# Optimization experiments

Measured on AMD Instinct MI355X. Metric: run time of the kernel, lower is better.

## Reference

```python
import jax, jax.numpy as jnp
import numpy as np

B, C, W, H = 2, 64, 96, 96  # N = W*H = 9216 spatial positions


def conv1x1(x, w, b):
    # x: (B, Cin, W, H), w: (Cout, Cin), b: (Cout,) -> (B, Cout, W, H)
    return jnp.einsum('bchw,oc->bohw', x, w) + b[None, :, None, None]


def setup_inputs() -> dict:
    key = jax.random.key(0)
    ks = jax.random.split(key, 4)
    c8 = C // 8
    s = 0.05  # small weight scale keeps softmax logits in a sane range
    return {
        'x': jax.random.normal(ks[0], (B, C, W, H), jnp.float32),
        'wq': jax.random.normal(ks[1], (c8, C), jnp.float32) * s,
        'bq': jnp.zeros((c8,), jnp.float32),
        'wk': jax.random.normal(ks[2], (c8, C), jnp.float32) * s,
        'bk': jnp.zeros((c8,), jnp.float32),
        'wv': jax.random.normal(ks[3], (C, C), jnp.float32) * s,
        'bv': jnp.zeros((C,), jnp.float32),
        'gamma': jnp.full((1,), 0.5, jnp.float32),
    }


def reference(x, wq, bq, wk, bk, wv, bv, gamma):
    b, c, w, h = x.shape
    n = w * h
    q = conv1x1(x, wq, bq).reshape(b, -1, n)   # (B, C//8, N)
    k = conv1x1(x, wk, bk).reshape(b, -1, n)   # (B, C//8, N)
    v = conv1x1(x, wv, bv).reshape(b, c, n)    # (B, C, N)
    energy = jnp.einsum('bci,bcj->bij', q, k)  # (B, N, N)
    attn = jax.nn.softmax(energy, axis=-1)
    # torch.bmm(v, attn): out[b,c,i] = sum_j v[b,c,j] * attn[b,j,i]
    out = jnp.einsum('bcj,bji->bci', v, attn).reshape(b, c, w, h)
    return gamma * out + x
```

## Files before the change

### kernel.cpp

```cpp
#include <hip/hip_runtime.h>

using half2v  = __attribute__((ext_vector_type(2))) _Float16;
using half4   = __attribute__((ext_vector_type(4))) _Float16;
using half8   = __attribute__((ext_vector_type(8))) _Float16;
using floatx4 = __attribute__((ext_vector_type(4))) float;

constexpr int BATCH = 2;
constexpr int NPOS  = 96 * 96;
constexpr int NT    = NPOS / 16;
constexpr int NST   = NPOS / 32;

#define EXP2(x) __builtin_amdgcn_exp2f(x)
#define MFMA16(A, B, C) __builtin_amdgcn_mfma_f32_16x16x16f16(A, B, C, 0, 0, 0)
#define MFMA32(A, B, C) __builtin_amdgcn_mfma_f32_16x16x32_f16(A, B, C, 0, 0, 0)

__device__ inline half8 p8_of(floatx4 e0, floatx4 e1) {
    half2v a0 = __builtin_bit_cast(half2v,
        __builtin_amdgcn_cvt_pkrtz(EXP2(e0[0]), EXP2(e0[1])));
    half2v a1 = __builtin_bit_cast(half2v,
        __builtin_amdgcn_cvt_pkrtz(EXP2(e0[2]), EXP2(e0[3])));
    half2v a2 = __builtin_bit_cast(half2v,
        __builtin_amdgcn_cvt_pkrtz(EXP2(e1[0]), EXP2(e1[1])));
    half2v a3 = __builtin_bit_cast(half2v,
        __builtin_amdgcn_cvt_pkrtz(EXP2(e1[2]), EXP2(e1[3])));
    half8 p = {a0[0], a0[1], a1[0], a1[1], a2[0], a2[1], a3[0], a3[1]};
    return p;
}

__global__ __launch_bounds__(256) void qkv_kernel(
    const float* __restrict__ x,
    const float* __restrict__ wq, const float* __restrict__ bq,
    const float* __restrict__ wk, const float* __restrict__ bk,
    const float* __restrict__ wv, const float* __restrict__ bv,
    _Float16* __restrict__ Qf, _Float16* __restrict__ Kf,
    _Float16* __restrict__ Vf)
{
    __shared__ float W[80][64];
    __shared__ float bias[80];
    __shared__ float qs[32][9];
    __shared__ float ks[32][9];
    __shared__ _Float16 vs[32][72];
    const int tid = threadIdx.x;
    for (int idx = tid; idx < 80 * 64; idx += 256) {
        int o = idx >> 6, c = idx & 63;
        float w;
        if (o < 8)       w = wq[o * 64 + c];
        else if (o < 16) w = wk[(o - 8) * 64 + c];
        else             w = wv[(o - 16) * 64 + c];
        W[o][c] = w;
    }
    if (tid < 80) {
        float bb;
        if (tid < 8)       bb = bq[tid];
        else if (tid < 16) bb = bk[tid - 8];
        else               bb = bv[tid - 16];
        bias[tid] = bb;
    }
    __syncthreads();

    const int js = blockIdx.x;
    const int b  = blockIdx.y;
    const int part = tid >> 5;
    const int jl   = tid & 31;
    const int i    = js * 32 + jl;

    float xr[64];
    #pragma unroll
    for (int c = 0; c < 64; ++c)
        xr[c] = x[(size_t)(b * 64 + c) * NPOS + i];

    #pragma unroll
    for (int q = 0; q < 10; ++q) {
        const int o = part * 10 + q;
        float s = bias[o];
        #pragma unroll
        for (int c4 = 0; c4 < 16; ++c4) {
            float4 w4 = *(const float4*)&W[o][c4 * 4];
            s += w4.x * xr[c4*4+0] + w4.y * xr[c4*4+1]
               + w4.z * xr[c4*4+2] + w4.w * xr[c4*4+3];
        }
        if (o < 8)       qs[jl][o] = s;
        else if (o < 16) ks[jl][o - 8] = s;
        else             vs[jl][o - 16] = (_Float16)s;
    }
    __syncthreads();

    const size_t tile = (size_t)b * NST + js;
    {
        const int ct = tid >> 6, l = tid & 63;
        const int g = l >> 4, cl = l & 15;
        half8 o8;
        #pragma unroll
        for (int idx = 0; idx < 8; ++idx)
            o8[idx] = vs[8 * g + idx][16 * ct + cl];
        *(half8*)&Vf[(tile * 256 + ct * 64 + l) * 8] = o8;
    }
    if (tid < 128) {
        const int l = tid >> 1, e = tid & 1;
        const int m = l & 15, g = l >> 4;
        const int jsrc = 8 * (m >> 2) + 4 * e + (m & 3);
        constexpr float LOG2E = 1.44269504088896f;
        half4 qh;
        #pragma unroll
        for (int r = 0; r < 4; ++r)
            qh[r] = (g < 2) ? (_Float16)(qs[jsrc][4 * g + r] * LOG2E)
                            : (_Float16)0.f;
        ((half4*)Qf)[(tile * 64 + l) * 2 + e] = qh;
    } else {
        const int t = tid - 128;
        const int ht = t >> 6, l = t & 63;
        const int il = l & 15, g = l >> 4;
        const int it = js * 2 + ht;
        half4 kh;
        #pragma unroll
        for (int r = 0; r < 4; ++r) {
            if (g < 2)       kh[r] = (_Float16)ks[16 * ht + il][4 * g + r];
            else if (g == 2) kh[r] = (r < 2) ? (_Float16)1.f : (_Float16)0.f;
            else             kh[r] = (_Float16)0.f;
        }
        ((half4*)Kf)[(size_t)(b * NT + it) * 64 + l] = kh;
    }
}

__global__ __launch_bounds__(256, 4) void denom_kernel(
    _Float16* __restrict__ Qf, const _Float16* __restrict__ Kf)
{
    __shared__ float LpS[4][32];
    const int tid = threadIdx.x;
    const int w = tid >> 6, l = tid & 63;
    const int js = blockIdx.x;
    const int b  = blockIdx.y;
    const size_t tile = (size_t)b * NST + js;
    const half8* __restrict__ qfb = (const half8*)Qf + (size_t)b * NST * 64;
    const half4* __restrict__ kfb = (const half4*)Kf + (size_t)b * NT * 64;

    half8 qv = qfb[(size_t)js * 64 + l];
    half4 q0 = __builtin_shufflevector(qv, qv, 0, 1, 2, 3);
    half4 q1 = __builtin_shufflevector(qv, qv, 4, 5, 6, 7);

    float sum[2][4];
    #pragma unroll
    for (int e = 0; e < 2; ++e)
        #pragma unroll
        for (int r = 0; r < 4; ++r) sum[e][r] = 0.f;

    const floatx4 z = {0.f, 0.f, 0.f, 0.f};
    #define DACC(E0, E1) do { \
        _Pragma("unroll") \
        for (int r = 0; r < 4; ++r) { \
            sum[0][r] += EXP2(E0[r]); sum[1][r] += EXP2(E1[r]); } \
    } while (0)

    const half4* kp = kfb + (size_t)w * 64 + l;
    half4 kfA = kp[0];
    half4 kfB = kp[256];
    floatx4 eA0 = MFMA16(q0, kfA, z), eA1 = MFMA16(q1, kfA, z);
    floatx4 eB0, eB1;
    for (int k = 0; k < 71; ++k) {
        kfA = kp[(size_t)(2 * k + 2) * 256];
        eB0 = MFMA16(q0, kfB, z); eB1 = MFMA16(q1, kfB, z);
        DACC(eA0, eA1);
        kfB = kp[(size_t)(2 * k + 3) * 256];
        eA0 = MFMA16(q0, kfA, z); eA1 = MFMA16(q1, kfA, z);
        DACC(eB0, eB1);
    }
    eB0 = MFMA16(q0, kfB, z); eB1 = MFMA16(q1, kfB, z);
    DACC(eA0, eA1);
    DACC(eB0, eB1);
    #undef DACC

    #pragma unroll
    for (int e = 0; e < 2; ++e)
        #pragma unroll
        for (int r = 0; r < 4; ++r)
            #pragma unroll
            for (int m = 1; m < 16; m <<= 1)
                sum[e][r] += __shfl_xor(sum[e][r], m, 64);

    if ((l & 15) == 0) {
        const int g = l >> 4;
        #pragma unroll
        for (int e = 0; e < 2; ++e)
            #pragma unroll
            for (int r = 0; r < 4; ++r)
                LpS[w][8 * g + 4 * e + r] = sum[e][r];
    }
    __syncthreads();

    if (tid < 32) {
        const float L = LpS[0][tid] + LpS[1][tid] + LpS[2][tid] + LpS[3][tid];
        const float v = -__log2f(L);
        _Float16 hi = (_Float16)v;
        _Float16 lo = (_Float16)(v - (float)hi);
        const int m = 4 * (tid >> 3) + (tid & 3);
        const int e = (tid >> 2) & 1;
        half2v hl = {hi, lo};
        ((half2v*)Qf)[((tile * 64 + m + 32) * 2 + e) * 2] = hl;
    }
}

__global__ __launch_bounds__(256, 2) void attn_kernel(
    const _Float16* __restrict__ Qf, const _Float16* __restrict__ Kf,
    const _Float16* __restrict__ Vf,
    const float* __restrict__ x, const float* __restrict__ gamma,
    float* __restrict__ out)
{
    __shared__ float red[4][3][64][17];
    const int s = blockIdx.x;
    const int b   = s & 1;
    const int igl = s >> 1;
    const int tid = threadIdx.x;
    const int w = tid >> 6, l = tid & 63;
    const int it0 = igl * 3, i0 = igl * 48;

    const half8* __restrict__ qfb = (const half8*)Qf + (size_t)b * NST * 64;
    const half4* __restrict__ kfb = (const half4*)Kf + (size_t)b * NT * 64;
    const half8* __restrict__ vfb = (const half8*)Vf + (size_t)b * NST * 256;

    half4 kf[3];
    #pragma unroll
    for (int st = 0; st < 3; ++st) kf[st] = kfb[(size_t)(it0 + st) * 64 + l];

    floatx4 acc[3][4];
    #pragma unroll
    for (int st = 0; st < 3; ++st)
        #pragma unroll
        for (int ct = 0; ct < 4; ++ct)
            acc[st][ct] = (floatx4){0.f, 0.f, 0.f, 0.f};

    const floatx4 z = {0.f, 0.f, 0.f, 0.f};

    #define ASTEP(QV, V0, V1, V2, V3) do { \
        half4 qe0 = __builtin_shufflevector(QV, QV, 0, 1, 2, 3); \
        half4 qe1 = __builtin_shufflevector(QV, QV, 4, 5, 6, 7); \
        _Pragma("unroll") \
        for (int st = 0; st < 3; ++st) { \
            floatx4 e0 = MFMA16(qe0, kf[st], z); \
            floatx4 e1 = MFMA16(qe1, kf[st], z); \
            half8 p = p8_of(e0, e1); \
            acc[st][0] = MFMA32(V0, p, acc[st][0]); \
            acc[st][1] = MFMA32(V1, p, acc[st][1]); \
            acc[st][2] = MFMA32(V2, p, acc[st][2]); \
            acc[st][3] = MFMA32(V3, p, acc[st][3]); \
        } \
    } while (0)

    const half8* qpw = qfb + (size_t)w * 64 + l;
    const half8* vpw = vfb + (size_t)w * 256 + l;

    half8 qv = qpw[0];
    half8 v0 = vpw[0], v1 = vpw[64], v2 = vpw[128], v3 = vpw[192];
    for (int k = 0; k < 71; ++k) {
        const size_t nx = (size_t)(k + 1);
        half8 qn  = qpw[nx * 256];
        half8 v0n = vpw[nx * 1024],       v1n = vpw[nx * 1024 + 64];
        half8 v2n = vpw[nx * 1024 + 128], v3n = vpw[nx * 1024 + 192];
        ASTEP(qv, v0, v1, v2, v3);
        qv = qn; v0 = v0n; v1 = v1n; v2 = v2n; v3 = v3n;
    }
    ASTEP(qv, v0, v1, v2, v3);
    #undef ASTEP

    #pragma unroll
    for (int st = 0; st < 3; ++st)
        #pragma unroll
        for (int ct = 0; ct < 4; ++ct)
            #pragma unroll
            for (int r = 0; r < 4; ++r)
                red[w][st][l][ct * 4 + r] = acc[st][ct][r];
    __syncthreads();

    if (w < 3) {
        const float g = gamma[0];
        const int iq = i0 + 16 * w + (l & 15);
        #pragma unroll
        for (int ct = 0; ct < 4; ++ct)
            #pragma unroll
            for (int r = 0; r < 4; ++r) {
                float v = red[0][w][l][ct*4+r] + red[1][w][l][ct*4+r]
                        + red[2][w][l][ct*4+r] + red[3][w][l][ct*4+r];
                int c = 16 * ct + 4 * (l >> 4) + r;
                size_t o = ((size_t)(b * 64 + c)) * NPOS + iq;
                out[o] = g * v + x[o];
            }
    }
}

extern "C" void kernel_launch(void* const* d_in, const int* in_sizes, int n_in,
                              void* d_out, int out_size, void* d_ws, size_t ws_size,
                              hipStream_t stream)
{
    const float* x     = (const float*)d_in[0];
    const float* wq    = (const float*)d_in[1];
    const float* bq    = (const float*)d_in[2];
    const float* wk    = (const float*)d_in[3];
    const float* bk    = (const float*)d_in[4];
    const float* wv    = (const float*)d_in[5];
    const float* bv    = (const float*)d_in[6];
    const float* gamma = (const float*)d_in[7];
    float* out = (float*)d_out;

    char* wsb = (char*)d_ws;
    _Float16* Qf = (_Float16*)wsb;
    _Float16* Kf = (_Float16*)(wsb + 589824);
    _Float16* Vf = (_Float16*)(wsb + 1179648);

    qkv_kernel<<<dim3(NST, BATCH), 256, 0, stream>>>(
        x, wq, bq, wk, bk, wv, bv, Qf, Kf, Vf);

    denom_kernel<<<dim3(NST, BATCH), 256, 0, stream>>>(Qf, Kf);

    attn_kernel<<<dim3(384), 256, 0, stream>>>(Qf, Kf, Vf, x, gamma, out);
}
```

Before: 144.6 us.

## Split attention key range across two blocks and combine partials in separate kernel

The attention kernel now splits the key/value sequence into two halves across a second grid dimension. Each half writes fp32 partial outputs to workspace, and a new combine kernel sums them and applies gamma and the residual. The denominator kernel also doubles its block to 512 threads (8 waves), so each wave covers half as many key tiles. This raises the number of blocks from 384 to 768 to fill more CUs, at the cost of an extra launch and extra global traffic for the partials. Launch bounds on the attention kernel are raised to 3 blocks per CU.

```diff
diff --git a/kernel.cpp b/kernel.cpp
--- a/kernel.cpp
+++ b/kernel.cpp
@@ -122,10 +122,10 @@
     }
 }
 
-__global__ __launch_bounds__(256, 4) void denom_kernel(
+__global__ __launch_bounds__(512, 4) void denom_kernel(
     _Float16* __restrict__ Qf, const _Float16* __restrict__ Kf)
 {
-    __shared__ float LpS[4][32];
+    __shared__ float LpS[8][32];
     const int tid = threadIdx.x;
     const int w = tid >> 6, l = tid & 63;
     const int js = blockIdx.x;
@@ -153,14 +153,14 @@
 
     const half4* kp = kfb + (size_t)w * 64 + l;
     half4 kfA = kp[0];
-    half4 kfB = kp[256];
+    half4 kfB = kp[512];
     floatx4 eA0 = MFMA16(q0, kfA, z), eA1 = MFMA16(q1, kfA, z);
     floatx4 eB0, eB1;
-    for (int k = 0; k < 71; ++k) {
-        kfA = kp[(size_t)(2 * k + 2) * 256];
+    for (int k = 0; k < 35; ++k) {
+        kfA = kp[(size_t)(2 * k + 2) * 512];
         eB0 = MFMA16(q0, kfB, z); eB1 = MFMA16(q1, kfB, z);
         DACC(eA0, eA1);
-        kfB = kp[(size_t)(2 * k + 3) * 256];
+        kfB = kp[(size_t)(2 * k + 3) * 512];
         eA0 = MFMA16(q0, kfA, z); eA1 = MFMA16(q1, kfA, z);
         DACC(eB0, eB1);
     }
@@ -188,7 +188,9 @@
     __syncthreads();
 
     if (tid < 32) {
-        const float L = LpS[0][tid] + LpS[1][tid] + LpS[2][tid] + LpS[3][tid];
+        float L = 0.f;
+        #pragma unroll
+        for (int u = 0; u < 8; ++u) L += LpS[u][tid];
         const float v = -__log2f(L);
         _Float16 hi = (_Float16)v;
         _Float16 lo = (_Float16)(v - (float)hi);
@@ -199,14 +201,14 @@
     }
 }
 
-__global__ __launch_bounds__(256, 2) void attn_kernel(
+__global__ __launch_bounds__(256, 3) void attn_kernel(
     const _Float16* __restrict__ Qf, const _Float16* __restrict__ Kf,
     const _Float16* __restrict__ Vf,
-    const float* __restrict__ x, const float* __restrict__ gamma,
-    float* __restrict__ out)
+    float* __restrict__ part)
 {
     __shared__ float red[4][3][64][17];
-    const int s = blockIdx.x;
+    const int s   = blockIdx.x;
+    const int jh  = blockIdx.y;
     const int b   = s & 1;
     const int igl = s >> 1;
     const int tid = threadIdx.x;
@@ -245,12 +247,13 @@
         } \
     } while (0)
 
-    const half8* qpw = qfb + (size_t)w * 64 + l;
-    const half8* vpw = vfb + (size_t)w * 256 + l;
+    const int st0 = jh * (NST / 2);
+    const half8* qpw = qfb + (size_t)(st0 + w) * 64 + l;
+    const half8* vpw = vfb + (size_t)(st0 + w) * 256 + l;
 
     half8 qv = qpw[0];
     half8 v0 = vpw[0], v1 = vpw[64], v2 = vpw[128], v3 = vpw[192];
-    for (int k = 0; k < 71; ++k) {
+    for (int k = 0; k < 35; ++k) {
         const size_t nx = (size_t)(k + 1);
         half8 qn  = qpw[nx * 256];
         half8 v0n = vpw[nx * 1024],       v1n = vpw[nx * 1024 + 64];
@@ -271,7 +274,8 @@
     __syncthreads();
 
     if (w < 3) {
-        const float g = gamma[0];
+        float* __restrict__ P =
+            part + (size_t)jh * ((size_t)BATCH * 64 * NPOS);
         const int iq = i0 + 16 * w + (l & 15);
         #pragma unroll
         for (int ct = 0; ct < 4; ++ct)
@@ -281,9 +285,28 @@
                         + red[2][w][l][ct*4+r] + red[3][w][l][ct*4+r];
                 int c = 16 * ct + 4 * (l >> 4) + r;
                 size_t o = ((size_t)(b * 64 + c)) * NPOS + iq;
-                out[o] = g * v + x[o];
+                P[o] = v;
             }
     }
+}
+
+__global__ __launch_bounds__(256) void combine_kernel(
+    const float* __restrict__ part, const float* __restrict__ x,
+    const float* __restrict__ gamma, float* __restrict__ out)
+{
+    const float g = gamma[0];
+    const size_t idx = (size_t)blockIdx.x * 256 + threadIdx.x;
+    const float4* p0 = (const float4*)part;
+    const float4* p1 = p0 + ((size_t)BATCH * 64 * NPOS) / 4;
+    float4 a  = p0[idx];
+    float4 c  = p1[idx];
+    float4 xv = ((const float4*)x)[idx];
+    float4 o;
+    o.x = g * (a.x + c.x) + xv.x;
+    o.y = g * (a.y + c.y) + xv.y;
+    o.z = g * (a.z + c.z) + xv.z;
+    o.w = g * (a.w + c.w) + xv.w;
+    ((float4*)out)[idx] = o;
 }
 
 extern "C" void kernel_launch(void* const* d_in, const int* in_sizes, int n_in,
@@ -304,11 +327,15 @@
     _Float16* Qf = (_Float16*)wsb;
     _Float16* Kf = (_Float16*)(wsb + 589824);
     _Float16* Vf = (_Float16*)(wsb + 1179648);
+    float*    Pp = (float*)(wsb + 3538944);
 
     qkv_kernel<<<dim3(NST, BATCH), 256, 0, stream>>>(
         x, wq, bq, wk, bk, wv, bv, Qf, Kf, Vf);
 
-    denom_kernel<<<dim3(NST, BATCH), 256, 0, stream>>>(Qf, Kf);
-
-    attn_kernel<<<dim3(384), 256, 0, stream>>>(Qf, Kf, Vf, x, gamma, out);
-}
+    denom_kernel<<<dim3(NST, BATCH), 512, 0, stream>>>(Qf, Kf);
+
+    attn_kernel<<<dim3(384, 2), 256, 0, stream>>>(Qf, Kf, Vf, Pp);
+
+    combine_kernel<<<(BATCH * 64 * NPOS / 4) / 256, 256, 0, stream>>>(
+        Pp, x, gamma, out);
+}
```

Result: faster. 138.7 us (-4.1%).
